# Kernel tuning notes

Hardware: AMD Instinct MI355X
Metric: run time of the kernel (lower is better)

## Reference

```python
import jax, jax.numpy as jnp
import numpy as np

N_NODES = 100000
N_ANCHORS = 32
EMB_DIM = 64


def setup_inputs() -> dict:
    key = jax.random.key(0)
    k1, k2, k3, k4, k5 = jax.random.split(key, 5)
    embeds = jax.random.normal(k1, (N_NODES, EMB_DIM), dtype=jnp.float32)
    dists_array = jax.random.uniform(k2, (N_NODES, N_ANCHORS), dtype=jnp.float32)
    # torch Linear(2*D, D): y = x @ W.T + b; we store W already transposed [2D, D]
    W_hidden = jax.random.normal(k3, (2 * EMB_DIM, EMB_DIM), dtype=jnp.float32) * (1.0 / np.sqrt(2 * EMB_DIM))
    b_hidden = jax.random.normal(k4, (EMB_DIM,), dtype=jnp.float32) * 0.01
    anchorset_id = jax.random.randint(k5, (N_ANCHORS,), 0, N_NODES)
    return {
        "embeds": embeds,
        "dists_array": dists_array,
        "W_hidden": W_hidden,
        "b_hidden": b_hidden,
        "anchorset_id": anchorset_id,
    }


def reference(embeds, dists_array, W_hidden, b_hidden, anchorset_id):
    # embeds: [N, D]; dists_array: [N, A]; anchorset_id: [A]
    set_emb = embeds[anchorset_id]                         # gather -> [A, D]
    msg_anchor = dists_array[:, :, None] * set_emb[None]   # [N, A, D]
    self_feat = jnp.broadcast_to(embeds[:, None, :], msg_anchor.shape)  # [N, A, D]
    messages = jnp.concatenate((msg_anchor, self_feat), axis=-1)        # [N, A, 2D]
    hidden = jnp.einsum('nae,ed->nad', messages, W_hidden) + b_hidden   # [N, A, D]
    return hidden.mean(axis=1)                              # [N, D]
```

## Files before the change

### kernel.cpp

```cpp
#include <hip/hip_runtime.h>
#include <cstdint>
#include <cstddef>


#define N_NODES 100000
#define DIM     64
#define NTILES  1563
#define GRID    768
#define AS_K    104

typedef short bf16x8 __attribute__((ext_vector_type(8)));
typedef float f32x4  __attribute__((ext_vector_type(4)));

__device__ __forceinline__ unsigned short f2bf(float f) {
    union { float f; unsigned u; } c; c.f = f;
    return (unsigned short)((c.u + 0x7fffu + ((c.u >> 16) & 1u)) >> 16);
}
__device__ __forceinline__ float bf2f(unsigned short h) {
    union { unsigned u; float f; } c; c.u = ((unsigned)h) << 16; return c.f;
}
__device__ __forceinline__ unsigned long long pack4h(float a, float b, float c, float d) {
    unsigned short h0 = f2bf(a), h1 = f2bf(b), h2 = f2bf(c), h3 = f2bf(d);
    return (unsigned long long)h0 | ((unsigned long long)h1 << 16) |
           ((unsigned long long)h2 << 32) | ((unsigned long long)h3 << 48);
}
__device__ __forceinline__ unsigned long long pack4l(float a, float b, float c, float d) {
    unsigned short l0 = f2bf(a - bf2f(f2bf(a))), l1 = f2bf(b - bf2f(f2bf(b)));
    unsigned short l2 = f2bf(c - bf2f(f2bf(c))), l3 = f2bf(d - bf2f(f2bf(d)));
    return (unsigned long long)l0 | ((unsigned long long)l1 << 16) |
           ((unsigned long long)l2 << 32) | ((unsigned long long)l3 << 48);
}

__global__ __launch_bounds__(256) void pnn_prep(
    const float* __restrict__ embeds, const float* __restrict__ W,
    const int* __restrict__ aid, unsigned short* __restrict__ fragB)
{
    const int b = blockIdx.x, tid = threadIdx.x;
    if (b < 8) {
        const int t = b * 256 + tid;
        const int a = t >> 6, d = t & 63;
        const float* se = embeds + (size_t)aid[a] * DIM;
        float s = 0.f;
        #pragma unroll
        for (int e = 0; e < DIM; ++e) s += se[e] * W[e * DIM + d];
        s *= (1.0f / 32.0f);
        const int j = a & 7, quad = a >> 3;
        const int nt = d >> 4, col = d & 15;
        const int lane = quad * 16 + col;
        const unsigned short hi = f2bf(s);
        fragB[((nt * 2 + 0) * 64 + lane) * 8 + j] = hi;
        fragB[((nt * 2 + 1) * 64 + lane) * 8 + j] = f2bf(s - bf2f(hi));
    } else {
        const int w = (b - 8) * 256 + tid;
        const int j    = w & 7;
        const int lane = (w >> 3) & 63;
        const int pl   = (w >> 9) & 1;
        const int nt   = (w >> 10) & 3;
        const int ks   = 1 + (w >> 12);
        const int k = ks * 32 + (lane >> 4) * 8 + j;
        const int n = nt * 16 + (lane & 15);
        const float v = W[(k + 32) * DIM + n];
        unsigned short h = f2bf(v);
        if (pl) h = f2bf(v - bf2f(h));
        fragB[(((ks * 4 + nt) * 2 + pl) * 64 + lane) * 8 + j] = h;
    }
}

#define LOAD_TILE(m0)                                                          \
    do {                                                                       \
        const float4* dg = (const float4*)(dists + (size_t)(m0) * 32);         \
        _Pragma("unroll")                                                      \
        for (int i = 0; i < 2; ++i) {                                          \
            const int f = i * 256 + tid;                                       \
            dv[i] = ((m0) + (f >> 3) < N_NODES) ? dg[f]                        \
                                                : make_float4(0.f,0.f,0.f,0.f);\
        }                                                                      \
        const float4* eg = (const float4*)(embeds + (size_t)(m0) * 64);        \
        _Pragma("unroll")                                                      \
        for (int i = 0; i < 4; ++i) {                                          \
            const int f = i * 256 + tid;                                       \
            ev[i] = ((m0) + (f >> 4) < N_NODES) ? eg[f]                        \
                                                : make_float4(0.f,0.f,0.f,0.f);\
        }                                                                      \
    } while (0)

__global__ __launch_bounds__(256, 3) void pnn_main(
    const float* __restrict__ embeds,
    const float* __restrict__ dists,
    const unsigned short* __restrict__ fragB,
    const float* __restrict__ bias,
    float* __restrict__ out)
{
    __shared__ __align__(16) unsigned short sB[12288];
    __shared__ __align__(16) unsigned short As[2][4][16][AS_K];

    const int tid  = threadIdx.x;
    const int wave = tid >> 6;
    const int lane = tid & 63;
    const int quad = lane >> 4;
    const int col  = lane & 15;

    #pragma unroll
    for (int i = 0; i < 6; ++i)
        ((uint4*)sB)[i * 256 + tid] = ((const uint4*)fragB)[i * 256 + tid];

    float bias_n[4];
    #pragma unroll
    for (int nt = 0; nt < 4; ++nt) bias_n[nt] = bias[nt * 16 + col];

    int tile = blockIdx.x;
    float4 dv[2], ev[4];
    LOAD_TILE(tile * 64);

    for (; tile < NTILES; tile += GRID) {
        const int n0 = tile * 64;

        #pragma unroll
        for (int i = 0; i < 2; ++i) {
            const int f  = i * 256 + tid;
            const int nd = f >> 3, k0 = (f & 7) * 4;
            const float4 v = dv[i];
            *(unsigned long long*)&As[0][nd >> 4][nd & 15][k0] = pack4h(v.x, v.y, v.z, v.w);
            *(unsigned long long*)&As[1][nd >> 4][nd & 15][k0] = pack4l(v.x, v.y, v.z, v.w);
        }
        #pragma unroll
        for (int i = 0; i < 4; ++i) {
            const int f  = i * 256 + tid;
            const int nd = f >> 4, k0 = 32 + (f & 15) * 4;
            const float4 v = ev[i];
            *(unsigned long long*)&As[0][nd >> 4][nd & 15][k0] = pack4h(v.x, v.y, v.z, v.w);
            *(unsigned long long*)&As[1][nd >> 4][nd & 15][k0] = pack4l(v.x, v.y, v.z, v.w);
        }
        __syncthreads();

        const int t2 = tile + GRID;
        if (t2 < NTILES) {
            LOAD_TILE(t2 * 64);
        }

        f32x4 acc[4];
        #pragma unroll
        for (int nt = 0; nt < 4; ++nt) {
            const float bb = bias_n[nt];
            acc[nt][0] = bb; acc[nt][1] = bb; acc[nt][2] = bb; acc[nt][3] = bb;
        }
        const bf16x8* Bl = (const bf16x8*)sB;
        #pragma unroll
        for (int ks = 0; ks < 3; ++ks) {
            const bf16x8 Ahi = *(const bf16x8*)&As[0][wave][col][ks * 32 + quad * 8];
            const bf16x8 Alo = *(const bf16x8*)&As[1][wave][col][ks * 32 + quad * 8];
            #pragma unroll
            for (int nt = 0; nt < 4; ++nt) {
                const bf16x8 Bh = Bl[((ks * 4 + nt) * 2 + 0) * 64 + lane];
                const bf16x8 Bo = Bl[((ks * 4 + nt) * 2 + 1) * 64 + lane];
                acc[nt] = __builtin_amdgcn_mfma_f32_16x16x32_bf16(Ahi, Bh, acc[nt], 0, 0, 0);
                acc[nt] = __builtin_amdgcn_mfma_f32_16x16x32_bf16(Ahi, Bo, acc[nt], 0, 0, 0);
                acc[nt] = __builtin_amdgcn_mfma_f32_16x16x32_bf16(Alo, Bh, acc[nt], 0, 0, 0);
            }
        }

        #pragma unroll
        for (int r = 0; r < 4; ++r) {
            const int node = n0 + wave * 16 + quad * 4 + r;
            if (node < N_NODES) {
                float* po = out + (size_t)node * DIM + col;
                #pragma unroll
                for (int nt = 0; nt < 4; ++nt) po[nt * 16] = acc[nt][r];
            }
        }
        __syncthreads();
    }
}

extern "C" void kernel_launch(void* const* d_in, const int* in_sizes, int n_in,
                              void* d_out, int out_size, void* d_ws, size_t ws_size,
                              hipStream_t stream) {
    const float* embeds = (const float*)d_in[0];
    const float* dists  = (const float*)d_in[1];
    const float* W      = (const float*)d_in[2];
    const float* bias   = (const float*)d_in[3];
    const int*   aid    = (const int*)d_in[4];
    float* out = (float*)d_out;

    unsigned short* fragB = (unsigned short*)d_ws;

    pnn_prep<<<40, 256, 0, stream>>>(embeds, W, aid, fragB);
    pnn_main<<<GRID, 256, 0, stream>>>(embeds, dists, fragB, bias, out);
}
```

Baseline: 95.31 us.

## Load A fragments directly from global into registers, one tile per block

```diff
diff --git a/kernel.cpp b/kernel.cpp
--- a/kernel.cpp
+++ b/kernel.cpp
@@ -6,8 +6,6 @@
 #define N_NODES 100000
 #define DIM     64
 #define NTILES  1563
-#define GRID    768
-#define AS_K    104
 
 typedef short bf16x8 __attribute__((ext_vector_type(8)));
 typedef float f32x4  __attribute__((ext_vector_type(4)));
@@ -29,6 +27,18 @@
     unsigned short l2 = f2bf(c - bf2f(f2bf(c))), l3 = f2bf(d - bf2f(f2bf(d)));
     return (unsigned long long)l0 | ((unsigned long long)l1 << 16) |
            ((unsigned long long)l2 << 32) | ((unsigned long long)l3 << 48);
+}
+__device__ __forceinline__ bf16x8 mk8h(float4 a, float4 b) {
+    union { unsigned long long u[2]; bf16x8 v; } t;
+    t.u[0] = pack4h(a.x, a.y, a.z, a.w);
+    t.u[1] = pack4h(b.x, b.y, b.z, b.w);
+    return t.v;
+}
+__device__ __forceinline__ bf16x8 mk8l(float4 a, float4 b) {
+    union { unsigned long long u[2]; bf16x8 v; } t;
+    t.u[0] = pack4l(a.x, a.y, a.z, a.w);
+    t.u[1] = pack4l(b.x, b.y, b.z, b.w);
+    return t.v;
 }
 
 __global__ __launch_bounds__(256) void pnn_prep(
@@ -66,25 +76,7 @@
     }
 }
 
-#define LOAD_TILE(m0)                                                          \
-    do {                                                                       \
-        const float4* dg = (const float4*)(dists + (size_t)(m0) * 32);         \
-        _Pragma("unroll")                                                      \
-        for (int i = 0; i < 2; ++i) {                                          \
-            const int f = i * 256 + tid;                                       \
-            dv[i] = ((m0) + (f >> 3) < N_NODES) ? dg[f]                        \
-                                                : make_float4(0.f,0.f,0.f,0.f);\
-        }                                                                      \
-        const float4* eg = (const float4*)(embeds + (size_t)(m0) * 64);        \
-        _Pragma("unroll")                                                      \
-        for (int i = 0; i < 4; ++i) {                                          \
-            const int f = i * 256 + tid;                                       \
-            ev[i] = ((m0) + (f >> 4) < N_NODES) ? eg[f]                        \
-                                                : make_float4(0.f,0.f,0.f,0.f);\
-        }                                                                      \
-    } while (0)
-
-__global__ __launch_bounds__(256, 3) void pnn_main(
+__global__ __launch_bounds__(256) void pnn_main(
     const float* __restrict__ embeds,
     const float* __restrict__ dists,
     const unsigned short* __restrict__ fragB,
@@ -92,83 +84,64 @@
     float* __restrict__ out)
 {
     __shared__ __align__(16) unsigned short sB[12288];
-    __shared__ __align__(16) unsigned short As[2][4][16][AS_K];
 
     const int tid  = threadIdx.x;
+
+    #pragma unroll
+    for (int i = 0; i < 6; ++i)
+        ((uint4*)sB)[i * 256 + tid] = ((const uint4*)fragB)[i * 256 + tid];
+    __syncthreads();
+
     const int wave = tid >> 6;
     const int lane = tid & 63;
     const int quad = lane >> 4;
     const int col  = lane & 15;
 
+    const int n0    = blockIdx.x * 64;
+    const int nodeA = n0 + wave * 16 + col;
+    const int nA    = nodeA < N_NODES ? nodeA : N_NODES - 1;
+
+    const float4* dp = (const float4*)(dists  + (size_t)nA * 32 + quad * 8);
+    const float4  d0 = dp[0], d1 = dp[1];
+    const float4* ep = (const float4*)(embeds + (size_t)nA * 64 + quad * 8);
+    const float4  f0 = ep[0], f1 = ep[1];
+    const float4* gp = (const float4*)(embeds + (size_t)nA * 64 + 32 + quad * 8);
+    const float4  g0 = gp[0], g1 = gp[1];
+
+    const bf16x8 Ahi0 = mk8h(d0, d1), Alo0 = mk8l(d0, d1);
+    const bf16x8 Ahi1 = mk8h(f0, f1), Alo1 = mk8l(f0, f1);
+    const bf16x8 Ahi2 = mk8h(g0, g1), Alo2 = mk8l(g0, g1);
+
+    f32x4 acc[4];
     #pragma unroll
-    for (int i = 0; i < 6; ++i)
-        ((uint4*)sB)[i * 256 + tid] = ((const uint4*)fragB)[i * 256 + tid];
+    for (int nt = 0; nt < 4; ++nt) {
+        const float bb = bias[nt * 16 + col];
+        acc[nt][0] = bb; acc[nt][1] = bb; acc[nt][2] = bb; acc[nt][3] = bb;
+    }
 
-    float bias_n[4];
+    const bf16x8* Bl = (const bf16x8*)sB;
     #pragma unroll
-    for (int nt = 0; nt < 4; ++nt) bias_n[nt] = bias[nt * 16 + col];
-
-    int tile = blockIdx.x;
-    float4 dv[2], ev[4];
-    LOAD_TILE(tile * 64);
-
-    for (; tile < NTILES; tile += GRID) {
-        const int n0 = tile * 64;
-
-        #pragma unroll
-        for (int i = 0; i < 2; ++i) {
-            const int f  = i * 256 + tid;
-            const int nd = f >> 3, k0 = (f & 7) * 4;
-            const float4 v = dv[i];
-            *(unsigned long long*)&As[0][nd >> 4][nd & 15][k0] = pack4h(v.x, v.y, v.z, v.w);
-            *(unsigned long long*)&As[1][nd >> 4][nd & 15][k0] = pack4l(v.x, v.y, v.z, v.w);
-        }
-        #pragma unroll
-        for (int i = 0; i < 4; ++i) {
-            const int f  = i * 256 + tid;
-            const int nd = f >> 4, k0 = 32 + (f & 15) * 4;
-            const float4 v = ev[i];
-            *(unsigned long long*)&As[0][nd >> 4][nd & 15][k0] = pack4h(v.x, v.y, v.z, v.w);
-            *(unsigned long long*)&As[1][nd >> 4][nd & 15][k0] = pack4l(v.x, v.y, v.z, v.w);
-        }
-        __syncthreads();
-
-        const int t2 = tile + GRID;
-        if (t2 < NTILES) {
-            LOAD_TILE(t2 * 64);
-        }
-
-        f32x4 acc[4];
+    for (int ks = 0; ks < 3; ++ks) {
+        const bf16x8 Ahi = (ks == 0) ? Ahi0 : (ks == 1) ? Ahi1 : Ahi2;
+        const bf16x8 Alo = (ks == 0) ? Alo0 : (ks == 1) ? Alo1 : Alo2;
         #pragma unroll
         for (int nt = 0; nt < 4; ++nt) {
-            const float bb = bias_n[nt];
-            acc[nt][0] = bb; acc[nt][1] = bb; acc[nt][2] = bb; acc[nt][3] = bb;
+            const bf16x8 Bh = Bl[((ks * 4 + nt) * 2 + 0) * 64 + lane];
+            const bf16x8 Bo = Bl[((ks * 4 + nt) * 2 + 1) * 64 + lane];
+            acc[nt] = __builtin_amdgcn_mfma_f32_16x16x32_bf16(Ahi, Bh, acc[nt], 0, 0, 0);
+            acc[nt] = __builtin_amdgcn_mfma_f32_16x16x32_bf16(Ahi, Bo, acc[nt], 0, 0, 0);
+            acc[nt] = __builtin_amdgcn_mfma_f32_16x16x32_bf16(Alo, Bh, acc[nt], 0, 0, 0);
         }
-        const bf16x8* Bl = (const bf16x8*)sB;
-        #pragma unroll
-        for (int ks = 0; ks < 3; ++ks) {
-            const bf16x8 Ahi = *(const bf16x8*)&As[0][wave][col][ks * 32 + quad * 8];
-            const bf16x8 Alo = *(const bf16x8*)&As[1][wave][col][ks * 32 + quad * 8];
+    }
+
+    #pragma unroll
+    for (int r = 0; r < 4; ++r) {
+        const int node = n0 + wave * 16 + quad * 4 + r;
+        if (node < N_NODES) {
+            float* po = out + (size_t)node * DIM + col;
             #pragma unroll
-            for (int nt = 0; nt < 4; ++nt) {
-                const bf16x8 Bh = Bl[((ks * 4 + nt) * 2 + 0) * 64 + lane];
-                const bf16x8 Bo = Bl[((ks * 4 + nt) * 2 + 1) * 64 + lane];
-                acc[nt] = __builtin_amdgcn_mfma_f32_16x16x32_bf16(Ahi, Bh, acc[nt], 0, 0, 0);
-                acc[nt] = __builtin_amdgcn_mfma_f32_16x16x32_bf16(Ahi, Bo, acc[nt], 0, 0, 0);
-                acc[nt] = __builtin_amdgcn_mfma_f32_16x16x32_bf16(Alo, Bh, acc[nt], 0, 0, 0);
-            }
+            for (int nt = 0; nt < 4; ++nt) po[nt * 16] = acc[nt][r];
         }
-
-        #pragma unroll
-        for (int r = 0; r < 4; ++r) {
-            const int node = n0 + wave * 16 + quad * 4 + r;
-            if (node < N_NODES) {
-                float* po = out + (size_t)node * DIM + col;
-                #pragma unroll
-                for (int nt = 0; nt < 4; ++nt) po[nt * 16] = acc[nt][r];
-            }
-        }
-        __syncthreads();
     }
 }
 
@@ -185,5 +158,5 @@
     unsigned short* fragB = (unsigned short*)d_ws;
 
     pnn_prep<<<40, 256, 0, stream>>>(embeds, W, aid, fragB);
-    pnn_main<<<GRID, 256, 0, stream>>>(embeds, dists, fragB, bias, out);
+    pnn_main<<<NTILES, 256, 0, stream>>>(embeds, dists, fragB, bias, out);
 }
```

Measured after the change: 95.44 us. About the same (+0.1%).
